# Optimization experiments

Measured on AMD Instinct MI355X. Metric: run time of the kernel, lower is better.

The kernel has to match this reference:

```python
import jax, jax.numpy as jnp
import numpy as np

B, L, ENC_D, DEC_D, ATTN_D = 64, 1024, 512, 512, 512


def setup_inputs() -> dict:
    key = jax.random.key(0)
    ks = jax.random.split(key, 8)
    s_enc = 1.0 / np.sqrt(ENC_D)
    s_dec = 1.0 / np.sqrt(DEC_D)
    s_att = 1.0 / np.sqrt(ATTN_D)
    return {
        "enc_out": jax.random.normal(ks[0], (B, L, ENC_D), dtype=jnp.float32),
        "dec_hidden": jax.random.normal(ks[1], (B, DEC_D), dtype=jnp.float32),
        # nn.Linear params (uniform(-1/sqrt(fan_in), 1/sqrt(fan_in)))
        "W_enc": jax.random.uniform(ks[2], (ENC_D, ATTN_D), jnp.float32, -s_enc, s_enc),
        "b_enc": jax.random.uniform(ks[3], (ATTN_D,), jnp.float32, -s_enc, s_enc),
        "W_dec": jax.random.uniform(ks[4], (DEC_D, ATTN_D), jnp.float32, -s_dec, s_dec),
        "b_dec": jax.random.uniform(ks[5], (ATTN_D,), jnp.float32, -s_dec, s_dec),
        "W_full": jax.random.uniform(ks[6], (ATTN_D,), jnp.float32, -s_att, s_att),
        "b_full": jax.random.uniform(ks[7], (), jnp.float32, -s_att, s_att),
    }


def reference(enc_out, dec_hidden, W_enc, b_enc, W_dec, b_dec, W_full, b_full):
    # attn1: [B, L, A]; attn2: [B, A]
    attn1 = jnp.einsum("ble,ea->bla", enc_out, W_enc) + b_enc
    attn2 = dec_hidden @ W_dec + b_dec
    # full_attn(relu(attn1 + attn2[:, None])) -> [B, L]
    attn = jnp.einsum("bla,a->bl", jax.nn.relu(attn1 + attn2[:, None, :]), W_full) + b_full
    alpha = jax.nn.softmax(attn, axis=1)  # over L
    attn_weighted_enc = jnp.einsum("ble,bl->be", enc_out, alpha)
    return attn_weighted_enc, alpha
```

## Files before the change

kernel.cpp:

```cpp
#include <hip/hip_runtime.h>
#include <hip/hip_bf16.h>

typedef __bf16 bf16x8 __attribute__((ext_vector_type(8)));
typedef float f32x4 __attribute__((ext_vector_type(4)));
typedef unsigned int u32;

#define B_SZ 64
#define L_SZ 1024
#define D_SZ 512

#define WS_WT     0
#define WS_BIAS   524288
#define WS_LOGITS 655360
#define WS_PART   917504

__device__ __forceinline__ unsigned short f2bf(float f) {
    __bf16 h = (__bf16)f;
    return __builtin_bit_cast(unsigned short, h);
}

__device__ __forceinline__ void gload_lds16(const void* g, void* l) {
    __builtin_amdgcn_global_load_lds(
        (const __attribute__((address_space(1))) u32*)g,
        (__attribute__((address_space(3))) u32*)l, 16, 0, 0);
}

__global__ void k_wt(const float* __restrict__ W, unsigned short* __restrict__ Wt) {
    int n = blockIdx.x;
    for (int k = threadIdx.x; k < 512; k += 256)
        Wt[n * 512 + k] = f2bf(W[k * 512 + n]);
}

__global__ void k_bias2(const float* __restrict__ dec, const float* __restrict__ Wd,
                        const float* __restrict__ b_dec, const float* __restrict__ b_enc,
                        float* __restrict__ bias2p) {
    int blk = blockIdx.x;
    int b = blk >> 2, nc = blk & 3;
    int t = threadIdx.x;
    __shared__ float sdec[512];
    __shared__ float red[256];
    for (int k = t; k < 512; k += 256) sdec[k] = dec[b * 512 + k];
    __syncthreads();
    int n = nc * 128 + (t & 127);
    int kh = t >> 7;
    float acc = 0.f;
    int k0 = kh * 256;
    #pragma unroll 4
    for (int k = k0; k < k0 + 256; ++k)
        acc += sdec[k] * Wd[k * 512 + n];
    red[t] = acc;
    __syncthreads();
    if (t < 128) {
        int nn = nc * 128 + t;
        bias2p[b * 512 + nn] = red[t] + red[t + 128] + b_dec[nn] + b_enc[nn];
    }
}

__global__ __launch_bounds__(256, 2) void k_logits(
        const float* __restrict__ enc, const unsigned short* __restrict__ Wt,
        const float* __restrict__ bias2p, const float* __restrict__ Wf,
        const float* __restrict__ bfull, float* __restrict__ logits) {
    __shared__ __align__(16) unsigned short lds[2][8192];

    int t = threadIdx.x;
    int lane = t & 63;
    int w = t >> 6;
    int blk = blockIdx.x;
    int rows0 = blk * 128;
    int b = blk >> 3;
    int m = lane & 15;
    int g = lane >> 4;

    bf16x8 A0[16], A1[16];
    {
        const float* ap0 = enc + (size_t)(rows0 + w * 32 + m) * 512 + g * 8;
        const float* ap1 = ap0 + 16 * 512;
        #pragma unroll
        for (int f = 0; f < 16; ++f) {
            float4 x = *(const float4*)(ap0 + f * 32);
            float4 y = *(const float4*)(ap0 + f * 32 + 4);
            bf16x8 a;
            a[0] = (__bf16)x.x; a[1] = (__bf16)x.y; a[2] = (__bf16)x.z; a[3] = (__bf16)x.w;
            a[4] = (__bf16)y.x; a[5] = (__bf16)y.y; a[6] = (__bf16)y.z; a[7] = (__bf16)y.w;
            A0[f] = a;
            float4 x1 = *(const float4*)(ap1 + f * 32);
            float4 y1 = *(const float4*)(ap1 + f * 32 + 4);
            bf16x8 a1;
            a1[0] = (__bf16)x1.x; a1[1] = (__bf16)x1.y; a1[2] = (__bf16)x1.z; a1[3] = (__bf16)x1.w;
            a1[4] = (__bf16)y1.x; a1[5] = (__bf16)y1.y; a1[6] = (__bf16)y1.z; a1[7] = (__bf16)y1.w;
            A1[f] = a1;
        }
    }

    #define STAGE(bufi, nc_)                                                      \
        {                                                                         \
            int n0_ = (nc_) * 16;                                                 \
            _Pragma("unroll")                                                     \
            for (int j = 0; j < 4; ++j) {                                         \
                int r_ = w * 4 + j;                                               \
                const char* src_ = (const char*)Wt + (size_t)(n0_ + r_) * 1024    \
                                   + ((lane ^ r_) << 4);                          \
                char* dst_ = (char*)&lds[bufi][0] + r_ * 1024;                    \
                gload_lds16(src_, dst_);                                          \
            }                                                                     \
        }

    STAGE(0, 0)
    __syncthreads();

    float p0[4] = {0.f, 0.f, 0.f, 0.f};
    float p1[4] = {0.f, 0.f, 0.f, 0.f};
    int buf = 0;
    int rbase = m * 1024;
    int swz = m << 4;

    for (int nc = 0; nc < 32; ++nc) {
        if (nc < 31) {
            if (buf) STAGE(0, nc + 1) else STAGE(1, nc + 1)
        }
        const char* base = (const char*)&lds[buf][0] + rbase;
        f32x4 acc0 = {0.f, 0.f, 0.f, 0.f};
        f32x4 acc1 = {0.f, 0.f, 0.f, 0.f};
        #pragma unroll
        for (int f = 0; f < 16; ++f) {
            uint4 raw = *(const uint4*)(base + ((f * 64 + g * 16) ^ swz));
            bf16x8 bfr = __builtin_bit_cast(bf16x8, raw);
            acc0 = __builtin_amdgcn_mfma_f32_16x16x32_bf16(A0[f], bfr, acc0, 0, 0, 0);
            acc1 = __builtin_amdgcn_mfma_f32_16x16x32_bf16(A1[f], bfr, acc1, 0, 0, 0);
        }
        int col = nc * 16 + m;
        float bias = bias2p[b * 512 + col];
        float wf = Wf[col];
        #pragma unroll
        for (int r = 0; r < 4; ++r) {
            float v0 = acc0[r] + bias; v0 = v0 > 0.f ? v0 : 0.f; p0[r] += v0 * wf;
            float v1 = acc1[r] + bias; v1 = v1 > 0.f ? v1 : 0.f; p1[r] += v1 * wf;
        }
        __syncthreads();
        buf ^= 1;
    }

    float bf0 = bfull[0];
    #pragma unroll
    for (int r = 0; r < 4; ++r) {
        float v = p0[r];
        v += __shfl_xor(v, 1, 64);
        v += __shfl_xor(v, 2, 64);
        v += __shfl_xor(v, 4, 64);
        v += __shfl_xor(v, 8, 64);
        if (m == 0) logits[rows0 + w * 32 + g * 4 + r] = v + bf0;
        float u = p1[r];
        u += __shfl_xor(u, 1, 64);
        u += __shfl_xor(u, 2, 64);
        u += __shfl_xor(u, 4, 64);
        u += __shfl_xor(u, 8, 64);
        if (m == 0) logits[rows0 + w * 32 + 16 + g * 4 + r] = u + bf0;
    }
}

__global__ void k_softmax(const float* __restrict__ logits, float* __restrict__ alpha) {
    int b = blockIdx.x;
    int t = threadIdx.x;
    __shared__ float red[256];
    float4 v = ((const float4*)(logits + b * 1024))[t];
    float mx = fmaxf(fmaxf(v.x, v.y), fmaxf(v.z, v.w));
    red[t] = mx;
    __syncthreads();
    for (int s = 128; s > 0; s >>= 1) {
        if (t < s) red[t] = fmaxf(red[t], red[t + s]);
        __syncthreads();
    }
    mx = red[0];
    __syncthreads();
    float4 e;
    e.x = expf(v.x - mx); e.y = expf(v.y - mx);
    e.z = expf(v.z - mx); e.w = expf(v.w - mx);
    red[t] = e.x + e.y + e.z + e.w;
    __syncthreads();
    for (int s = 128; s > 0; s >>= 1) {
        if (t < s) red[t] += red[t + s];
        __syncthreads();
    }
    float inv = 1.0f / red[0];
    float4 o;
    o.x = e.x * inv; o.y = e.y * inv; o.z = e.z * inv; o.w = e.w * inv;
    ((float4*)(alpha + b * 1024))[t] = o;
}

__global__ void k_wsum_part(const float* __restrict__ enc, const float* __restrict__ alpha,
                            float* __restrict__ part) {
    int blk = blockIdx.x;
    int b = blk >> 3, c = blk & 7;
    int t = threadIdx.x;
    const float* ep = enc + (size_t)(b * 1024 + c * 128) * 512;
    const float* al = alpha + b * 1024 + c * 128;
    float ax = 0.f, ay = 0.f;
    #pragma unroll 4
    for (int l = 0; l < 128; ++l) {
        float a = al[l];
        float2 e = *(const float2*)(ep + (size_t)l * 512 + t * 2);
        ax += e.x * a;
        ay += e.y * a;
    }
    float* pp = part + (size_t)blk * 512;
    pp[t * 2] = ax;
    pp[t * 2 + 1] = ay;
}

__global__ void k_wsum_final(const float* __restrict__ part, float* __restrict__ out) {
    int b = blockIdx.x;
    int t = threadIdx.x;
    float sx = 0.f, sy = 0.f;
    #pragma unroll
    for (int c = 0; c < 8; ++c) {
        float2 v = *(const float2*)(part + (size_t)(b * 8 + c) * 512 + t * 2);
        sx += v.x;
        sy += v.y;
    }
    float2 o; o.x = sx; o.y = sy;
    *(float2*)(out + b * 512 + t * 2) = o;
}

extern "C" void kernel_launch(void* const* d_in, const int* in_sizes, int n_in,
                              void* d_out, int out_size, void* d_ws, size_t ws_size,
                              hipStream_t stream) {
    const float* enc    = (const float*)d_in[0];
    const float* dec    = (const float*)d_in[1];
    const float* W_enc  = (const float*)d_in[2];
    const float* b_enc  = (const float*)d_in[3];
    const float* W_dec  = (const float*)d_in[4];
    const float* b_dec  = (const float*)d_in[5];
    const float* W_full = (const float*)d_in[6];
    const float* b_full = (const float*)d_in[7];

    float* out = (float*)d_out;
    char* ws = (char*)d_ws;
    unsigned short* Wt = (unsigned short*)(ws + WS_WT);
    float* bias2p = (float*)(ws + WS_BIAS);
    float* logits = (float*)(ws + WS_LOGITS);
    float* part   = (float*)(ws + WS_PART);
    float* alpha  = out + 32768;

    hipLaunchKernelGGL(k_wt,         dim3(512), dim3(256), 0, stream, W_enc, Wt);
    hipLaunchKernelGGL(k_bias2,      dim3(256), dim3(256), 0, stream, dec, W_dec, b_dec, b_enc, bias2p);
    hipLaunchKernelGGL(k_logits,     dim3(512), dim3(256), 0, stream, enc, Wt, bias2p, W_full, b_full, logits);
    hipLaunchKernelGGL(k_softmax,    dim3(64),  dim3(256), 0, stream, logits, alpha);
    hipLaunchKernelGGL(k_wsum_part,  dim3(512), dim3(256), 0, stream, enc, alpha, part);
    hipLaunchKernelGGL(k_wsum_final, dim3(64),  dim3(256), 0, stream, part, out);
}
```

Before: 109.6 us.

## Split logits K dimension across wave pairs and vectorize weighted-sum kernels

The logits kernel now runs 512 threads per block: each pair of waves splits the 512-wide reduction dimension in half and combines partial MFMA accumulators through shared memory. This halves the per-thread A-fragment registers so more waves fit per CU, at the cost of an extra barrier and LDS round-trip per column chunk. The weighted-sum kernels switch to float4 loads with two row halves reduced in shared memory, and the final reduction uses 128 threads with float4.

```diff
diff --git a/kernel.cpp b/kernel.cpp
--- a/kernel.cpp
+++ b/kernel.cpp
@@ -56,27 +56,43 @@
     }
 }
 
-__global__ __launch_bounds__(256, 2) void k_logits(
+__global__ __launch_bounds__(512, 4) void k_logits(
         const float* __restrict__ enc, const unsigned short* __restrict__ Wt,
         const float* __restrict__ bias2p, const float* __restrict__ Wf,
         const float* __restrict__ bfull, float* __restrict__ logits) {
     __shared__ __align__(16) unsigned short lds[2][8192];
+    __shared__ f32x4 comb[4][2][64];
 
     int t = threadIdx.x;
     int lane = t & 63;
     int w = t >> 6;
+    int rg = w >> 1;
+    int h = w & 1;
     int blk = blockIdx.x;
-    int rows0 = blk * 128;
     int b = blk >> 3;
     int m = lane & 15;
     int g = lane >> 4;
 
-    bf16x8 A0[16], A1[16];
+    #define STAGE(bufi, nc_)                                                      \
+        {                                                                         \
+            int n0_ = (nc_) * 16;                                                 \
+            _Pragma("unroll")                                                     \
+            for (int j = 0; j < 2; ++j) {                                         \
+                int c_ = w * 2 + j;                                               \
+                const char* src_ = (const char*)Wt + (size_t)(n0_ + c_) * 1024    \
+                                   + ((lane ^ c_) << 4);                          \
+                gload_lds16(src_, (char*)&lds[bufi][0] + c_ * 1024);              \
+            }                                                                     \
+        }
+
+    STAGE(0, 0)
+
+    bf16x8 A0[8], A1[8];
     {
-        const float* ap0 = enc + (size_t)(rows0 + w * 32 + m) * 512 + g * 8;
+        const float* ap0 = enc + (size_t)(blk * 128 + rg * 32 + m) * 512 + h * 256 + g * 8;
         const float* ap1 = ap0 + 16 * 512;
         #pragma unroll
-        for (int f = 0; f < 16; ++f) {
+        for (int f = 0; f < 8; ++f) {
             float4 x = *(const float4*)(ap0 + f * 32);
             float4 y = *(const float4*)(ap0 + f * 32 + 4);
             bf16x8 a;
@@ -92,69 +108,65 @@
         }
     }
 
-    #define STAGE(bufi, nc_)                                                      \
-        {                                                                         \
-            int n0_ = (nc_) * 16;                                                 \
-            _Pragma("unroll")                                                     \
-            for (int j = 0; j < 4; ++j) {                                         \
-                int r_ = w * 4 + j;                                               \
-                const char* src_ = (const char*)Wt + (size_t)(n0_ + r_) * 1024    \
-                                   + ((lane ^ r_) << 4);                          \
-                char* dst_ = (char*)&lds[bufi][0] + r_ * 1024;                    \
-                gload_lds16(src_, dst_);                                          \
-            }                                                                     \
-        }
-
-    STAGE(0, 0)
     __syncthreads();
 
     float p0[4] = {0.f, 0.f, 0.f, 0.f};
     float p1[4] = {0.f, 0.f, 0.f, 0.f};
-    int buf = 0;
-    int rbase = m * 1024;
     int swz = m << 4;
 
     for (int nc = 0; nc < 32; ++nc) {
+        int buf = nc & 1;
         if (nc < 31) {
             if (buf) STAGE(0, nc + 1) else STAGE(1, nc + 1)
         }
-        const char* base = (const char*)&lds[buf][0] + rbase;
+        const char* base = (const char*)&lds[buf][0] + m * 1024;
         f32x4 acc0 = {0.f, 0.f, 0.f, 0.f};
         f32x4 acc1 = {0.f, 0.f, 0.f, 0.f};
         #pragma unroll
-        for (int f = 0; f < 16; ++f) {
-            uint4 raw = *(const uint4*)(base + ((f * 64 + g * 16) ^ swz));
+        for (int f = 0; f < 8; ++f) {
+            uint4 raw = *(const uint4*)(base + (((h * 8 + f) * 64 + g * 16) ^ swz));
             bf16x8 bfr = __builtin_bit_cast(bf16x8, raw);
             acc0 = __builtin_amdgcn_mfma_f32_16x16x32_bf16(A0[f], bfr, acc0, 0, 0, 0);
             acc1 = __builtin_amdgcn_mfma_f32_16x16x32_bf16(A1[f], bfr, acc1, 0, 0, 0);
         }
-        int col = nc * 16 + m;
-        float bias = bias2p[b * 512 + col];
-        float wf = Wf[col];
+        if (h == 1) {
+            comb[rg][0][lane] = acc0;
+            comb[rg][1][lane] = acc1;
+        }
+        __syncthreads();
+        if (h == 0) {
+            f32x4 c0 = comb[rg][0][lane];
+            f32x4 c1 = comb[rg][1][lane];
+            int col = nc * 16 + m;
+            float bias = bias2p[b * 512 + col];
+            float wf = Wf[col];
+            #pragma unroll
+            for (int r = 0; r < 4; ++r) {
+                float v0 = acc0[r] + c0[r] + bias; v0 = v0 > 0.f ? v0 : 0.f; p0[r] += v0 * wf;
+                float v1 = acc1[r] + c1[r] + bias; v1 = v1 > 0.f ? v1 : 0.f; p1[r] += v1 * wf;
+            }
+        }
+        __syncthreads();
+    }
+
+    if (h == 0) {
+        float bf0 = bfull[0];
+        int rowbase = blk * 128 + rg * 32;
         #pragma unroll
         for (int r = 0; r < 4; ++r) {
-            float v0 = acc0[r] + bias; v0 = v0 > 0.f ? v0 : 0.f; p0[r] += v0 * wf;
-            float v1 = acc1[r] + bias; v1 = v1 > 0.f ? v1 : 0.f; p1[r] += v1 * wf;
-        }
-        __syncthreads();
-        buf ^= 1;
-    }
-
-    float bf0 = bfull[0];
-    #pragma unroll
-    for (int r = 0; r < 4; ++r) {
-        float v = p0[r];
-        v += __shfl_xor(v, 1, 64);
-        v += __shfl_xor(v, 2, 64);
-        v += __shfl_xor(v, 4, 64);
-        v += __shfl_xor(v, 8, 64);
-        if (m == 0) logits[rows0 + w * 32 + g * 4 + r] = v + bf0;
-        float u = p1[r];
-        u += __shfl_xor(u, 1, 64);
-        u += __shfl_xor(u, 2, 64);
-        u += __shfl_xor(u, 4, 64);
-        u += __shfl_xor(u, 8, 64);
-        if (m == 0) logits[rows0 + w * 32 + 16 + g * 4 + r] = u + bf0;
+            float v = p0[r];
+            v += __shfl_xor(v, 1, 64);
+            v += __shfl_xor(v, 2, 64);
+            v += __shfl_xor(v, 4, 64);
+            v += __shfl_xor(v, 8, 64);
+            if (m == 0) logits[rowbase + g * 4 + r] = v + bf0;
+            float u = p1[r];
+            u += __shfl_xor(u, 1, 64);
+            u += __shfl_xor(u, 2, 64);
+            u += __shfl_xor(u, 4, 64);
+            u += __shfl_xor(u, 8, 64);
+            if (m == 0) logits[rowbase + 16 + g * 4 + r] = u + bf0;
+        }
     }
 }
 
@@ -192,33 +204,41 @@
     int blk = blockIdx.x;
     int b = blk >> 3, c = blk & 7;
     int t = threadIdx.x;
+    int col = (t & 127) * 4;
+    int lh = t >> 7;
     const float* ep = enc + (size_t)(b * 1024 + c * 128) * 512;
     const float* al = alpha + b * 1024 + c * 128;
-    float ax = 0.f, ay = 0.f;
+    float4 s = {0.f, 0.f, 0.f, 0.f};
     #pragma unroll 4
-    for (int l = 0; l < 128; ++l) {
+    for (int i = 0; i < 64; ++i) {
+        int l = i * 2 + lh;
         float a = al[l];
-        float2 e = *(const float2*)(ep + (size_t)l * 512 + t * 2);
-        ax += e.x * a;
-        ay += e.y * a;
-    }
-    float* pp = part + (size_t)blk * 512;
-    pp[t * 2] = ax;
-    pp[t * 2 + 1] = ay;
+        float4 e = *(const float4*)(ep + (size_t)l * 512 + col);
+        s.x += e.x * a; s.y += e.y * a; s.z += e.z * a; s.w += e.w * a;
+    }
+    __shared__ float red[2][512];
+    *(float4*)&red[lh][col] = s;
+    __syncthreads();
+    if (t < 128) {
+        float4 a0 = *(const float4*)&red[0][t * 4];
+        float4 a1 = *(const float4*)&red[1][t * 4];
+        float4 o;
+        o.x = a0.x + a1.x; o.y = a0.y + a1.y;
+        o.z = a0.z + a1.z; o.w = a0.w + a1.w;
+        *(float4*)(part + (size_t)blk * 512 + t * 4) = o;
+    }
 }
 
 __global__ void k_wsum_final(const float* __restrict__ part, float* __restrict__ out) {
     int b = blockIdx.x;
     int t = threadIdx.x;
-    float sx = 0.f, sy = 0.f;
+    float4 s = {0.f, 0.f, 0.f, 0.f};
     #pragma unroll
     for (int c = 0; c < 8; ++c) {
-        float2 v = *(const float2*)(part + (size_t)(b * 8 + c) * 512 + t * 2);
-        sx += v.x;
-        sy += v.y;
-    }
-    float2 o; o.x = sx; o.y = sy;
-    *(float2*)(out + b * 512 + t * 2) = o;
+        float4 v = *(const float4*)(part + (size_t)(b * 8 + c) * 512 + t * 4);
+        s.x += v.x; s.y += v.y; s.z += v.z; s.w += v.w;
+    }
+    *(float4*)(out + b * 512 + t * 4) = s;
 }
 
 extern "C" void kernel_launch(void* const* d_in, const int* in_sizes, int n_in,
@@ -243,8 +263,8 @@
 
     hipLaunchKernelGGL(k_wt,         dim3(512), dim3(256), 0, stream, W_enc, Wt);
     hipLaunchKernelGGL(k_bias2,      dim3(256), dim3(256), 0, stream, dec, W_dec, b_dec, b_enc, bias2p);
-    hipLaunchKernelGGL(k_logits,     dim3(512), dim3(256), 0, stream, enc, Wt, bias2p, W_full, b_full, logits);
+    hipLaunchKernelGGL(k_logits,     dim3(512), dim3(512), 0, stream, enc, Wt, bias2p, W_full, b_full, logits);
     hipLaunchKernelGGL(k_softmax,    dim3(64),  dim3(256), 0, stream, logits, alpha);
     hipLaunchKernelGGL(k_wsum_part,  dim3(512), dim3(256), 0, stream, enc, alpha, part);
-    hipLaunchKernelGGL(k_wsum_final, dim3(64),  dim3(256), 0, stream, part, out);
-}
+    hipLaunchKernelGGL(k_wsum_final, dim3(64),  dim3(128), 0, stream, part, out);
+}
```

New measurement: 112.8 us. 3.0% more time.
